# Performance work log

Measured on AMD Instinct MI355X. Metric: run time of the kernel, lower is better.

Reference implementation:

```python
import jax, jax.numpy as jnp
import numpy as np

MIN_TEMPERATURE = 1e-8
MIN_PROB = 1e-10
NEG_INF = float('-inf')


def setup_inputs() -> dict:
    key = jax.random.key(0)
    k1, k2, k3, k4, k5 = jax.random.split(key, 5)
    B, V = 128, 128256
    logits = jax.random.normal(k1, (B, V), dtype=jnp.float32)
    temperatures = jax.random.uniform(k2, (B,), dtype=jnp.float32)
    top_ps = jax.random.uniform(k3, (B,), dtype=jnp.float32)
    top_ks = jax.random.randint(k4, (B,), 0, 1024, dtype=jnp.int64)
    min_ps = jax.random.uniform(k5, (B,), dtype=jnp.float32)
    return {"logits": logits, "temperatures": temperatures, "top_ps": top_ps,
            "top_ks": top_ks, "min_ps": min_ps}


def reference(logits, temperatures, top_ps, top_ks, min_ps):
    B, V = logits.shape
    rows = jnp.arange(B)[:, None]

    temps = jnp.maximum(temperatures, MIN_TEMPERATURE)
    original_scaled = logits.astype(jnp.float32) / temps[:, None]
    x = original_scaled

    # ---- top-k filter (rank-based; equivalent to torch.topk + scatter mask) ----
    order_k = jnp.argsort(-x, axis=-1)            # [B,V] token ids sorted desc
    ranks = jnp.argsort(order_k, axis=-1)         # rank of each token in its row
    keep_topk = ranks < top_ks[:, None]
    active_k = (top_ks > 0) & (top_ks < V)
    keep_topk = jnp.where(active_k[:, None], keep_topk, True)
    x = jnp.where(keep_topk, x, NEG_INF)

    # ---- top-p (nucleus) filter ----
    probs = jax.nn.softmax(x, axis=-1)
    order_p = jnp.argsort(-probs, axis=-1)
    sorted_probs = jnp.take_along_axis(probs, order_p, axis=-1)
    cum = jnp.cumsum(sorted_probs, axis=-1)
    remove_sorted = cum > top_ps[:, None]
    # shift right so the first token above the threshold is kept
    remove_sorted = jnp.concatenate(
        [jnp.zeros((B, 1), dtype=bool), remove_sorted[:, :-1]], axis=-1)
    remove = jnp.zeros((B, V), dtype=bool).at[rows, order_p].set(remove_sorted)
    x = jnp.where(remove, NEG_INF, x)

    # ---- min-p filter ----
    probs = jax.nn.softmax(x, axis=-1)
    top_prob = jnp.max(probs, axis=-1, keepdims=True)
    x = jnp.where(probs < min_ps[:, None] * top_prob, NEG_INF, x)

    # ---- fallback if everything got filtered ----
    all_filtered = jnp.all(jnp.isneginf(x), axis=-1)
    x = jnp.where(all_filtered[:, None], original_scaled, x)

    # ---- final softmax with nan guard + renormalize ----
    probs = jax.nn.softmax(x, axis=-1)
    probs = jnp.nan_to_num(probs, nan=0.0)
    probs = probs / jnp.maximum(jnp.sum(probs, axis=-1, keepdims=True), MIN_PROB)

    # ---- multinomial sample (1 draw per row) ----
    tokens = jax.random.categorical(jax.random.key(42), jnp.log(probs), axis=-1)
    return tokens
```

## Files before the change

### kernel.cpp

```cpp
#include <hip/hip_runtime.h>


#define TPS 512
#define TPB 1024
#define VOC 128256
#define V4 (VOC / 4)
#define NBINS 2048
#define CAPG 2048
#define TIE_CAP 1024
#define IMAXI 0x7fffffff
#define FIXS 1.7592186044416e13
#define THRK 0xC0100000u

#define WS_CNT 0
#define WS_CAP 512

__device__ __forceinline__ unsigned fkey(float x) {
  unsigned b = __float_as_uint(x);
  return b ^ ((b & 0x80000000u) ? 0xFFFFFFFFu : 0x80000000u);
}
__device__ __forceinline__ float keyf(unsigned k) {
  unsigned b = (k & 0x80000000u) ? (k ^ 0x80000000u) : ~k;
  return __uint_as_float(b);
}
__device__ __forceinline__ unsigned rotl32(unsigned v, int r) {
  return (v << r) | (v >> (32 - r));
}

__device__ __forceinline__ float gumbel_at(unsigned i) {
  const unsigned ks1 = 42u;
  const unsigned ks2 = 0x1BD11BDAu ^ 42u;
  unsigned x0 = 0u;
  unsigned x1 = i + ks1;
  x0 += x1; x1 = rotl32(x1, 13); x1 ^= x0;
  x0 += x1; x1 = rotl32(x1, 15); x1 ^= x0;
  x0 += x1; x1 = rotl32(x1, 26); x1 ^= x0;
  x0 += x1; x1 = rotl32(x1, 6);  x1 ^= x0;
  x0 += ks1; x1 += ks2 + 1u;
  x0 += x1; x1 = rotl32(x1, 17); x1 ^= x0;
  x0 += x1; x1 = rotl32(x1, 29); x1 ^= x0;
  x0 += x1; x1 = rotl32(x1, 16); x1 ^= x0;
  x0 += x1; x1 = rotl32(x1, 24); x1 ^= x0;
  x0 += ks2; x1 += 0u + 2u;
  x0 += x1; x1 = rotl32(x1, 13); x1 ^= x0;
  x0 += x1; x1 = rotl32(x1, 15); x1 ^= x0;
  x0 += x1; x1 = rotl32(x1, 26); x1 ^= x0;
  x0 += x1; x1 = rotl32(x1, 6);  x1 ^= x0;
  x0 += 0u; x1 += ks1 + 3u;
  x0 += x1; x1 = rotl32(x1, 17); x1 ^= x0;
  x0 += x1; x1 = rotl32(x1, 29); x1 ^= x0;
  x0 += x1; x1 = rotl32(x1, 16); x1 ^= x0;
  x0 += x1; x1 = rotl32(x1, 24); x1 ^= x0;
  x0 += ks1; x1 += ks2 + 4u;
  x0 += x1; x1 = rotl32(x1, 13); x1 ^= x0;
  x0 += x1; x1 = rotl32(x1, 15); x1 ^= x0;
  x0 += x1; x1 = rotl32(x1, 26); x1 ^= x0;
  x0 += x1; x1 = rotl32(x1, 6);  x1 ^= x0;
  x0 += ks2; x1 += 0u + 5u;
  unsigned bits = x0 ^ x1;
  unsigned fb = (bits >> 9) | 0x3f800000u;
  float f = __uint_as_float(fb) - 1.0f;
  float u = (f > 0.0f) ? f : 1.17549435e-38f;
  return -logf(-logf(u));
}

__device__ __forceinline__ void scan32g(unsigned* H, int n, int tid, int tpb) {
  for (int d = 1; d < n; d <<= 1) {
    unsigned v[4]; int c = 0;
    for (int i = tid; i < n; i += tpb) {
      v[c] = H[i] + ((i + d < n) ? H[i + d] : 0u);
      ++c;
    }
    __syncthreads();
    c = 0;
    for (int i = tid; i < n; i += tpb) { H[i] = v[c]; ++c; }
    __syncthreads();
  }
}
__device__ __forceinline__ void scan64(unsigned long long* H, int n, int tid) {
  for (int d = 1; d < n; d <<= 1) {
    unsigned long long v0 = 0ull, v1 = 0ull;
    int i0 = tid, i1 = tid + TPB;
    bool a0 = (i0 < n), a1 = (i1 < n);
    if (a0) { v0 = H[i0]; if (i0 + d < n) v0 += H[i0 + d]; }
    if (a1) { v1 = H[i1]; if (i1 + d < n) v1 += H[i1 + d]; }
    __syncthreads();
    if (a0) H[i0] = v0;
    if (a1) H[i1] = v1;
    __syncthreads();
  }
}

#define FOR_ALL(...)                                                          \
  for (int c_ = 0; c_ < 32; ++c_) {                                           \
    const int i4_ = c_ * TPB + tid;                                           \
    if (i4_ < V4) {                                                           \
      const float4 L_ = ((const float4*)rowp)[i4_];                           \
      const float xs_[4] = { L_.x / tclamp, L_.y / tclamp,                    \
                             L_.z / tclamp, L_.w / tclamp };                  \
      const int base_ = i4_ * 4;                                              \
      for (int j_ = 0; j_ < 4; ++j_) {                                        \
        const int idx = base_ + j_; const float x = xs_[j_];                  \
        __VA_ARGS__                                                           \
      }                                                                       \
    }                                                                         \
  }

extern "C" __global__ void __launch_bounds__(TPS)
k3_capture(const float* __restrict__ logits, const float* __restrict__ temps,
           unsigned char* __restrict__ ws)
{
  __shared__ unsigned long long Ls[CAPG];
  __shared__ unsigned sh_nloc, sh_base;
  const int blk = blockIdx.x, row = blk >> 3, sb = blk & 7;
  const int tid = threadIdx.x;
  const float* rowp = logits + (size_t)row * VOC;
  const float tclamp = fmaxf(temps[row], 1e-8f);
  if (tid == 0) sh_nloc = 0u;
  __syncthreads();
  for (int c = 0; c < 8; ++c) {
    const int i4 = c * 4096 + sb * TPS + tid;
    if (i4 < V4) {
      const float4 L = ((const float4*)rowp)[i4];
      const float v[4] = { L.x, L.y, L.z, L.w };
      const int base = i4 * 4;
      for (int j = 0; j < 4; ++j) {
        if (fkey(v[j]) >= THRK) {
          float x = v[j] / tclamp;
          unsigned kx = fkey(x);
          unsigned p = atomicAdd(&sh_nloc, 1u);
          if (p < CAPG)
            Ls[p] = ((unsigned long long)(~kx) << 32) | (unsigned)(base + j);
        }
      }
    }
  }
  __syncthreads();
  const unsigned nloc = sh_nloc;
  if (tid == 0) {
    unsigned res = (nloc > CAPG) ? (unsigned)(CAPG + 1) : nloc;
    sh_base = atomicAdd(&((unsigned*)(ws + WS_CNT))[row], res);
  }
  __syncthreads();
  const unsigned base = sh_base;
  const unsigned nw = min(nloc, (unsigned)CAPG);
  unsigned long long* cap = (unsigned long long*)(ws + WS_CAP) + (size_t)row * CAPG;
  for (unsigned i = tid; i < nw; i += TPS) {
    unsigned q = base + i;
    if (q < CAPG) cap[q] = Ls[i];
  }
}

extern "C" __global__ void __launch_bounds__(TPB)
k4_sample(const float* __restrict__ logits, const float* __restrict__ temps,
          const float* __restrict__ topps, const int* __restrict__ topks,
          const float* __restrict__ minps, const unsigned char* __restrict__ ws,
          int* __restrict__ out)
{
  __shared__ unsigned long long A[CAPG];
  __shared__ unsigned Hc[NBINS];
  __shared__ double D[TPB];
  __shared__ float redw[16];
  __shared__ int   redi[16];
  __shared__ double redd[16];
  __shared__ float sh_m;
  __shared__ int sh_b0, sh_b1, sh_b2;
  __shared__ unsigned sh_above;
  __shared__ unsigned long long sh_ab64;
  __shared__ int sh_p, sh_tn, sh_I2;
  __shared__ double sh_Z3;

  const int tid = threadIdx.x;
  const int row = blockIdx.x;
  const float* rowp = logits + (size_t)row * VOC;
  const float tclamp = fmaxf(temps[row], 1e-8f);
  const float topp = topps[row];
  const float minp = minps[row];
  const int k = topks[row];
  const bool ka = (k > 0) && (k < VOC);
  const int n = (int)((const unsigned*)(ws + WS_CNT))[row];

  if (ka && k <= TPB && n >= k && n <= CAPG) {
    const unsigned long long* capr =
        (const unsigned long long*)(ws + WS_CAP) + (size_t)row * CAPG;
    for (int i = tid; i < n; i += TPB) A[i] = capr[i];
    int S = 2; while (S < n) S <<= 1;
    for (int i = n + tid; i < S; i += TPB) A[i] = ~0ull;
    for (int size = 2; size <= S; size <<= 1)
      for (int stride = size >> 1; stride > 0; stride >>= 1) {
        __syncthreads();
        for (int i = tid; i < S; i += TPB) {
          int j = i ^ stride;
          if (j > i) {
            unsigned long long a = A[i], b = A[j];
            bool up = ((i & size) == 0);
            if ((a > b) == up) { A[i] = b; A[j] = a; }
          }
        }
      }
    __syncthreads();
    const float m = keyf(~(unsigned)(A[0] >> 32));
    unsigned idx_i = 0u; float e_i = 0.0f;
    const bool valid = (tid < k);
    if (valid) {
      unsigned long long a = A[tid];
      idx_i = (unsigned)a;
      e_i = expf(keyf(~(unsigned)(a >> 32)) - m);
    }
    double v = valid ? (double)e_i : 0.0;
    for (int o = 1; o < 64; o <<= 1) {
      double t = __shfl_up(v, o);
      if ((tid & 63) >= o) v += t;
    }
    if ((tid & 63) == 63) redd[tid >> 6] = v;
    __syncthreads();
    if (tid == 0) {
      double acc = 0.0;
      for (int w = 0; w < 16; ++w) { double t = redd[w]; redd[w] = acc; acc += t; }
    }
    __syncthreads();
    v += redd[tid >> 6];
    D[tid] = v;
    __syncthreads();
    const double Z1 = D[k - 1];
    const double T = (double)topp * Z1;
    if (tid == 0) sh_p = 0;
    __syncthreads();
    if (valid) {
      bool kept = (tid == 0) || (D[tid - 1] <= T);
      if (kept) atomicMax(&sh_p, tid);
    }
    __syncthreads();
    const int p2 = sh_p + 1;
    const float Z2f = (float)D[p2 - 1];
    const float e0 = expf(0.0f);
    const float thrm = minp * (e0 / Z2f);
    __syncthreads();
    if (tid == 0) sh_p = 0;
    __syncthreads();
    if (valid && tid < p2) {
      float q = e_i / Z2f;
      if (!(q < thrm)) atomicMax(&sh_p, tid);
    }
    __syncthreads();
    const int p3 = sh_p + 1;
    const float Z3f = (float)D[p3 - 1];
    float bw = -INFINITY; int bi = IMAXI;
    if (valid && tid < p3) {
      bw = logf(e_i / Z3f) + gumbel_at((unsigned)row * (unsigned)VOC + idx_i);
      bi = (int)idx_i;
    }
    for (int o = 32; o > 0; o >>= 1) {
      float ow = __shfl_down(bw, o);
      int   oi = __shfl_down(bi, o);
      if (ow > bw || (ow == bw && oi < bi)) { bw = ow; bi = oi; }
    }
    if ((tid & 63) == 0) { redw[tid >> 6] = bw; redi[tid >> 6] = bi; }
    __syncthreads();
    if (tid == 0) {
      float w = redw[0]; int ii = redi[0];
      for (int i = 1; i < 16; ++i)
        if (redw[i] > w || (redw[i] == w && redi[i] < ii)) { w = redw[i]; ii = redi[i]; }
      out[row] = ii;
    }
    return;
  }

  {
    float lmax = -INFINITY;
    FOR_ALL( (void)idx; lmax = fmaxf(lmax, x); )
    for (int o = 32; o > 0; o >>= 1) lmax = fmaxf(lmax, __shfl_down(lmax, o));
    if ((tid & 63) == 0) redw[tid >> 6] = lmax;
    __syncthreads();
    if (tid == 0) {
      float mm = redw[0];
      for (int i = 1; i < 16; ++i) mm = fmaxf(mm, redw[i]);
      sh_m = mm;
    }
    __syncthreads();
  }
  const float m = sh_m;

  unsigned tk_key = 0u; int rem_k = 0;
  if (ka) {
    for (int i = tid; i < NBINS; i += TPB) Hc[i] = 0u;
    __syncthreads();
    FOR_ALL( (void)idx; atomicAdd(&Hc[fkey(x) >> 21], 1u); )
    __syncthreads();
    scan32g(Hc, NBINS, tid, TPB);
    unsigned kku = (unsigned)k;
    for (int i = tid; i < NBINS; i += TPB) {
      unsigned hi = Hc[i], hn = (i + 1 < NBINS) ? Hc[i + 1] : 0u;
      if (hi >= kku && hn < kku) { sh_b0 = i; sh_above = hn; }
    }
    __syncthreads();
    const int b0 = sh_b0; kku -= sh_above;
    __syncthreads();
    for (int i = tid; i < NBINS; i += TPB) Hc[i] = 0u;
    __syncthreads();
    FOR_ALL(
      (void)idx;
      unsigned key = fkey(x);
      if ((int)(key >> 21) == b0) atomicAdd(&Hc[(key >> 10) & 0x7FFu], 1u);
    )
    __syncthreads();
    scan32g(Hc, NBINS, tid, TPB);
    for (int i = tid; i < NBINS; i += TPB) {
      unsigned hi = Hc[i], hn = (i + 1 < NBINS) ? Hc[i + 1] : 0u;
      if (hi >= kku && hn < kku) { sh_b1 = i; sh_above = hn; }
    }
    __syncthreads();
    const int b1 = sh_b1; kku -= sh_above;
    __syncthreads();
    for (int i = tid; i < NBINS; i += TPB) Hc[i] = 0u;
    __syncthreads();
    const unsigned pathk = ((unsigned)b0 << 11) | (unsigned)b1;
    FOR_ALL(
      (void)idx;
      unsigned key = fkey(x);
      if ((key >> 10) == pathk) atomicAdd(&Hc[key & 0x3FFu], 1u);
    )
    __syncthreads();
    scan32g(Hc, 1024, tid, TPB);
    for (int i = tid; i < 1024; i += TPB) {
      unsigned hi = Hc[i], hn = (i + 1 < 1024) ? Hc[i + 1] : 0u;
      if (hi >= kku && hn < kku) { sh_b2 = i; sh_above = hn; }
    }
    __syncthreads();
    rem_k = (int)(kku - sh_above);
    tk_key = ((unsigned)b0 << 21) | ((unsigned)b1 << 10) | (unsigned)sh_b2;
    __syncthreads();
  }
  const bool hk = ka;
  const float e_tk = hk ? expf(keyf(tk_key) - m) : 0.0f;
  const unsigned long long e_tk_fix = (unsigned long long)((double)e_tk * FIXS);
  unsigned long long* H = A;
  for (int i = tid; i < NBINS; i += TPB) H[i] = 0ull;
  __syncthreads();
  FOR_ALL(
    (void)idx;
    unsigned key = fkey(x);
    if (!hk || key > tk_key) {
      float e = expf(x - m);
      unsigned long long ef = (unsigned long long)((double)e * FIXS);
      if (ef) atomicAdd(&H[key >> 21], ef);
    }
  )
  __syncthreads();
  if (tid == 0 && hk) H[tk_key >> 21] += (unsigned long long)(unsigned)rem_k * e_tk_fix;
  __syncthreads();
  scan64(H, NBINS, tid);
  const unsigned long long Z1fix = H[0];
  const unsigned long long Tfix = (unsigned long long)((double)topp * (double)Z1fix);
  const int keepall = (Z1fix <= Tfix);

  unsigned t2_key = 0u; int rem2 = 0, all_mode = 0;
  double Z2d = 0.0; float e_t = 0.0f;

  if (!keepall) {
    for (int i = tid; i < NBINS; i += TPB) {
      unsigned long long hi = H[i], hn = (i + 1 < NBINS) ? H[i + 1] : 0ull;
      if (hi > Tfix && hn <= Tfix) { sh_b0 = i; sh_ab64 = hn; }
    }
    __syncthreads();
    const int b0p = sh_b0;
    const unsigned long long S0 = sh_ab64;
    __syncthreads();
    for (int i = tid; i < NBINS; i += TPB) H[i] = 0ull;
    __syncthreads();
    FOR_ALL(
      (void)idx;
      unsigned key = fkey(x);
      if ((int)(key >> 21) == b0p && (!hk || key > tk_key)) {
        float e = expf(x - m);
        unsigned long long ef = (unsigned long long)((double)e * FIXS);
        if (ef) atomicAdd(&H[(key >> 10) & 0x7FFu], ef);
      }
    )
    __syncthreads();
    if (tid == 0 && hk && (int)(tk_key >> 21) == b0p)
      H[(tk_key >> 10) & 0x7FFu] += (unsigned long long)(unsigned)rem_k * e_tk_fix;
    __syncthreads();
    scan64(H, NBINS, tid);
    {
      const unsigned long long T1 = Tfix - S0;
      for (int i = tid; i < NBINS; i += TPB) {
        unsigned long long hi = H[i], hn = (i + 1 < NBINS) ? H[i + 1] : 0ull;
        if (hi > T1 && hn <= T1) { sh_b1 = i; sh_ab64 = hn; }
      }
    }
    __syncthreads();
    const int b1p = sh_b1;
    const unsigned long long S1 = S0 + sh_ab64;
    __syncthreads();
    for (int i = tid; i < NBINS; i += TPB) H[i] = 0ull;
    for (int i = tid; i < 1024; i += TPB) Hc[i] = 0u;
    __syncthreads();
    const unsigned pathp = ((unsigned)b0p << 11) | (unsigned)b1p;
    FOR_ALL(
      (void)idx;
      unsigned key = fkey(x);
      if ((key >> 10) == pathp && (!hk || key > tk_key)) {
        float e = expf(x - m);
        unsigned long long ef = (unsigned long long)((double)e * FIXS);
        atomicAdd(&H[key & 0x3FFu], ef);
        atomicAdd(&Hc[key & 0x3FFu], 1u);
      }
    )
    __syncthreads();
    if (tid == 0 && hk && (tk_key >> 10) == pathp) {
      H[tk_key & 0x3FFu] += (unsigned long long)(unsigned)rem_k * e_tk_fix;
      Hc[tk_key & 0x3FFu] += (unsigned)rem_k;
    }
    __syncthreads();
    scan64(H, 1024, tid);
    {
      const unsigned long long T2 = Tfix - S1;
      for (int i = tid; i < 1024; i += TPB) {
        unsigned long long hi = H[i], hn = (i + 1 < 1024) ? H[i + 1] : 0ull;
        if (hi > T2 && hn <= T2) { sh_b2 = i; sh_ab64 = hn; }
      }
    }
    __syncthreads();
    const int b2p = sh_b2;
    const unsigned long long Sfix = S1 + sh_ab64;
    t2_key = ((unsigned)b0p << 21) | ((unsigned)b1p << 10) | (unsigned)b2p;
    const int c_t2 = (int)Hc[b2p];
    e_t = expf(keyf(t2_key) - m);
    const double Td = (double)topp * ((double)Z1fix / FIXS);
    const double Sd = (double)Sfix / FIXS;
    const double jmd = (Td - Sd) / (double)e_t;
    int rem_p;
    if (jmd >= (double)c_t2) rem_p = c_t2;
    else {
      rem_p = (int)jmd + 1;
      if (rem_p > c_t2) rem_p = c_t2;
      if (rem_p < 1) rem_p = 1;
    }
    rem2 = rem_p;
    const unsigned long long Z2fix =
        Sfix + (unsigned long long)(unsigned)rem_p *
                   (unsigned long long)((double)e_t * FIXS);
    Z2d = (double)Z2fix / FIXS;
  } else {
    if (hk) { t2_key = tk_key; rem2 = rem_k; e_t = e_tk; }
    else    { all_mode = 1; }
    Z2d = (double)Z1fix / FIXS;
  }

  if (tid == 0) { sh_tn = 0; sh_I2 = IMAXI; }
  __syncthreads();
  const float Z2f = (float)Z2d;
  const float thrm = minp * (1.0f / Z2f);
  double zp = 0.0;
  FOR_ALL(
    unsigned key = fkey(x);
    if (all_mode || key > t2_key) {
      float e = expf(x - m);
      float q1 = e / Z2f;
      if (!(q1 < thrm)) zp += (double)e;
    } else if (key == t2_key) {
      int p = atomicAdd(&sh_tn, 1);
      if (p < TIE_CAP) Hc[p] = (unsigned)idx;
    }
  )
  for (int o = 32; o > 0; o >>= 1) zp += __shfl_down(zp, o);
  if ((tid & 63) == 0) redd[tid >> 6] = zp;
  __syncthreads();
  int class_ok = 1;
  if (!all_mode) { float q1t = e_t / Z2f; class_ok = !(q1t < thrm); }
  if (tid == 0) {
    double z3 = 0.0;
    for (int i = 0; i < 16; ++i) z3 += redd[i];
    if (!all_mode && class_ok) z3 += (double)rem2 * (double)e_t;
    sh_Z3 = z3;
  }
  __syncthreads();
  const int tn = sh_tn;
  if (!all_mode && rem2 < tn && tn <= TIE_CAP) {
    if (tid < tn) {
      unsigned mine = Hc[tid];
      int r = 0;
      for (int j = 0; j < tn; ++j) r += (Hc[j] < mine);
      if (r == rem2 - 1) sh_I2 = (int)mine;
    }
  }
  __syncthreads();
  const int I2 = sh_I2;
  const float Z3f = (float)sh_Z3;
  float bw = -INFINITY; int bi = IMAXI;
  FOR_ALL(
    unsigned key = fkey(x);
    bool kp = all_mode || key > t2_key || (key == t2_key && idx <= I2);
    if (kp) {
      float e = expf(x - m);
      float q1 = e / Z2f;
      if (!(q1 < thrm)) {
        float w = logf(e / Z3f) + gumbel_at((unsigned)row * (unsigned)VOC + (unsigned)idx);
        if (w > bw) { bw = w; bi = idx; }
        else if (w == bw && idx < bi) bi = idx;
      }
    }
  )
  for (int o = 32; o > 0; o >>= 1) {
    float ow = __shfl_down(bw, o);
    int   oi = __shfl_down(bi, o);
    if (ow > bw || (ow == bw && oi < bi)) { bw = ow; bi = oi; }
  }
  if ((tid & 63) == 0) { redw[tid >> 6] = bw; redi[tid >> 6] = bi; }
  __syncthreads();
  if (tid == 0) {
    float w = redw[0]; int ii = redi[0];
    for (int i = 1; i < 16; ++i)
      if (redw[i] > w || (redw[i] == w && redi[i] < ii)) { w = redw[i]; ii = redi[i]; }
    out[row] = ii;
  }
}

extern "C" void kernel_launch(void* const* d_in, const int* in_sizes, int n_in,
                              void* d_out, int out_size, void* d_ws, size_t ws_size,
                              hipStream_t stream) {
  (void)n_in; (void)ws_size; (void)out_size;
  const float* logits = (const float*)d_in[0];
  const float* temps  = (const float*)d_in[1];
  const float* topps  = (const float*)d_in[2];
  const int*   topks  = (const int*)d_in[3];
  const float* minps  = (const float*)d_in[4];
  int* out = (int*)d_out;
  const int rows = in_sizes[1];
  unsigned char* ws = (unsigned char*)d_ws;
  hipMemsetAsync(ws + WS_CNT, 0, rows * sizeof(unsigned), stream);
  k3_capture<<<dim3(rows * 8), dim3(TPS), 0, stream>>>(logits, temps, ws);
  k4_sample<<<dim3(rows), dim3(TPB), 0, stream>>>(logits, temps, topps, topks,
                                                  minps, ws, out);
}
```

Baseline: 138.9 us.

## Use per-segment capture slots and warp-shuffle bitonic sort, drop memset

Each capture block now writes its candidates to a fixed per-segment slot with its own count, which removes the global atomic and the memset launch. The sample kernel computes segment offsets and gathers the candidates. It then sorts a fixed 2048-entry buffer with bitonic merges, using wave-level shuffles for strides below 64 so fewer block-wide barriers are needed. The trade-offs are a fixed-size sort even when n is small, and a fallback to the slow path when any segment exceeds 320 candidates.

Measured after the change: 125.9 us (median of 2 runs). 1.1x faster.

```diff
diff --git a/kernel.cpp b/kernel.cpp
--- a/kernel.cpp
+++ b/kernel.cpp
@@ -6,14 +6,16 @@
 #define VOC 128256
 #define V4 (VOC / 4)
 #define NBINS 2048
-#define CAPG 2048
+#define SEG 320
+#define CAPROW (8 * SEG)
+#define CAP2 2048
 #define TIE_CAP 1024
 #define IMAXI 0x7fffffff
 #define FIXS 1.7592186044416e13
 #define THRK 0xC0100000u
 
 #define WS_CNT 0
-#define WS_CAP 512
+#define WS_CAP 4096
 
 __device__ __forceinline__ unsigned fkey(float x) {
   unsigned b = __float_as_uint(x);
@@ -64,6 +66,18 @@
   return -logf(-logf(u));
 }
 
+__device__ __forceinline__ unsigned long long bmerge(
+    unsigned long long v, int i, int size, int maxs) {
+  const bool up = ((i & size) == 0);
+  for (int s = maxs; s > 0; s >>= 1) {
+    unsigned long long p = __shfl_xor(v, s, 64);
+    bool keep_min = (up == ((i & s) == 0));
+    bool take = keep_min ? (p < v) : (p > v);
+    if (take) v = p;
+  }
+  return v;
+}
+
 __device__ __forceinline__ void scan32g(unsigned* H, int n, int tid, int tpb) {
   for (int d = 1; d < n; d <<= 1) {
     unsigned v[4]; int c = 0;
@@ -110,8 +124,8 @@
 k3_capture(const float* __restrict__ logits, const float* __restrict__ temps,
            unsigned char* __restrict__ ws)
 {
-  __shared__ unsigned long long Ls[CAPG];
-  __shared__ unsigned sh_nloc, sh_base;
+  __shared__ unsigned long long Ls[SEG];
+  __shared__ unsigned sh_nloc;
   const int blk = blockIdx.x, row = blk >> 3, sb = blk & 7;
   const int tid = threadIdx.x;
   const float* rowp = logits + (size_t)row * VOC;
@@ -129,7 +143,7 @@
           float x = v[j] / tclamp;
           unsigned kx = fkey(x);
           unsigned p = atomicAdd(&sh_nloc, 1u);
-          if (p < CAPG)
+          if (p < SEG)
             Ls[p] = ((unsigned long long)(~kx) << 32) | (unsigned)(base + j);
         }
       }
@@ -137,18 +151,11 @@
   }
   __syncthreads();
   const unsigned nloc = sh_nloc;
-  if (tid == 0) {
-    unsigned res = (nloc > CAPG) ? (unsigned)(CAPG + 1) : nloc;
-    sh_base = atomicAdd(&((unsigned*)(ws + WS_CNT))[row], res);
-  }
-  __syncthreads();
-  const unsigned base = sh_base;
-  const unsigned nw = min(nloc, (unsigned)CAPG);
-  unsigned long long* cap = (unsigned long long*)(ws + WS_CAP) + (size_t)row * CAPG;
-  for (unsigned i = tid; i < nw; i += TPS) {
-    unsigned q = base + i;
-    if (q < CAPG) cap[q] = Ls[i];
-  }
+  if (tid == 0) ((unsigned*)(ws + WS_CNT))[row * 8 + sb] = nloc;
+  unsigned long long* cap = (unsigned long long*)(ws + WS_CAP) +
+                            (size_t)row * CAPROW + (size_t)sb * SEG;
+  const unsigned nw = min(nloc, (unsigned)SEG);
+  for (unsigned i = tid; i < nw; i += TPS) cap[i] = Ls[i];
 }
 
 extern "C" __global__ void __launch_bounds__(TPB)
@@ -157,12 +164,14 @@
           const float* __restrict__ minps, const unsigned char* __restrict__ ws,
           int* __restrict__ out)
 {
-  __shared__ unsigned long long A[CAPG];
+  __shared__ unsigned long long A[CAP2];
   __shared__ unsigned Hc[NBINS];
   __shared__ double D[TPB];
   __shared__ float redw[16];
   __shared__ int   redi[16];
   __shared__ double redd[16];
+  __shared__ int segoff[9];
+  __shared__ int sh_bad;
   __shared__ float sh_m;
   __shared__ int sh_b0, sh_b1, sh_b2;
   __shared__ unsigned sh_above;
@@ -178,27 +187,63 @@
   const float minp = minps[row];
   const int k = topks[row];
   const bool ka = (k > 0) && (k < VOC);
-  const int n = (int)((const unsigned*)(ws + WS_CNT))[row];
-
-  if (ka && k <= TPB && n >= k && n <= CAPG) {
+
+  if (tid == 0) {
+    const unsigned* cnts = (const unsigned*)(ws + WS_CNT) + row * 8;
+    int acc = 0, bad = 0;
+    for (int b = 0; b < 8; ++b) {
+      segoff[b] = acc;
+      unsigned c = cnts[b];
+      if (c > SEG) bad = 1;
+      acc += (int)c;
+    }
+    segoff[8] = acc;
+    sh_bad = bad;
+  }
+  __syncthreads();
+  const int n = segoff[8];
+
+  if (ka && k <= TPB && !sh_bad && n >= k && n <= CAP2) {
     const unsigned long long* capr =
-        (const unsigned long long*)(ws + WS_CAP) + (size_t)row * CAPG;
-    for (int i = tid; i < n; i += TPB) A[i] = capr[i];
-    int S = 2; while (S < n) S <<= 1;
-    for (int i = n + tid; i < S; i += TPB) A[i] = ~0ull;
-    for (int size = 2; size <= S; size <<= 1)
-      for (int stride = size >> 1; stride > 0; stride >>= 1) {
-        __syncthreads();
-        for (int i = tid; i < S; i += TPB) {
-          int j = i ^ stride;
+        (const unsigned long long*)(ws + WS_CAP) + (size_t)row * CAPROW;
+    for (int b = 0; b < 8; ++b) {
+      const int off = segoff[b], cnt = segoff[b + 1] - off;
+      for (int i = tid; i < cnt; i += TPB) A[off + i] = capr[b * SEG + i];
+    }
+    for (int i = n + tid; i < CAP2; i += TPB) A[i] = ~0ull;
+    __syncthreads();
+    const int lane = tid & 63, wave = tid >> 6;
+    for (int g = wave; g < 32; g += 16) {
+      const int i = g * 64 + lane;
+      unsigned long long v = A[i];
+      v = bmerge(v, i, 2, 1);
+      v = bmerge(v, i, 4, 2);
+      v = bmerge(v, i, 8, 4);
+      v = bmerge(v, i, 16, 8);
+      v = bmerge(v, i, 32, 16);
+      v = bmerge(v, i, 64, 32);
+      A[i] = v;
+    }
+    __syncthreads();
+    for (int size = 128; size <= CAP2; size <<= 1) {
+      for (int stride = size >> 1; stride >= 64; stride >>= 1) {
+        for (int r = 0; r < 2; ++r) {
+          const int i = tid + (r << 10);
+          const int j = i ^ stride;
           if (j > i) {
             unsigned long long a = A[i], b = A[j];
             bool up = ((i & size) == 0);
             if ((a > b) == up) { A[i] = b; A[j] = a; }
           }
         }
-      }
-    __syncthreads();
+        __syncthreads();
+      }
+      for (int g = wave; g < 32; g += 16) {
+        const int i = g * 64 + lane;
+        A[i] = bmerge(A[i], i, size, 32);
+      }
+      __syncthreads();
+    }
     const float m = keyf(~(unsigned)(A[0] >> 32));
     unsigned idx_i = 0u; float e_i = 0.0f;
     const bool valid = (tid < k);
@@ -529,7 +574,6 @@
   int* out = (int*)d_out;
   const int rows = in_sizes[1];
   unsigned char* ws = (unsigned char*)d_ws;
-  hipMemsetAsync(ws + WS_CNT, 0, rows * sizeof(unsigned), stream);
   k3_capture<<<dim3(rows * 8), dim3(TPS), 0, stream>>>(logits, temps, ws);
   k4_sample<<<dim3(rows), dim3(TPB), 0, stream>>>(logits, temps, topps, topks,
                                                   minps, ws, out);
```
